# Kernel optimization log

Hardware: AMD Instinct MI355X
Metric: run time of the kernel (lower is better)

## Reference

```python
import jax, jax.numpy as jnp
import numpy as np
import math

HEADS = 4
LN_EPS = 1e-5


def _layer_norm(x, gamma, beta):
    # LayerNorm over last dim (N=4096), matching nn.LayerNorm(4096)
    mu = jnp.mean(x, axis=-1, keepdims=True)
    var = jnp.mean((x - mu) ** 2, axis=-1, keepdims=True)
    return (x - mu) * jax.lax.rsqrt(var + LN_EPS) * gamma + beta


def setup_inputs() -> dict:
    key = jax.random.key(0)
    ks = jax.random.split(key, 10)
    L, IMG, N = 1024, 1024, 4096
    s_img = 1.0 / math.sqrt(IMG)
    s_L = 1.0 / math.sqrt(L)
    return {
        "point_features": jax.random.normal(ks[0], (1, L, N), jnp.float32),
        "img_features": jax.random.normal(ks[1], (1, IMG, N), jnp.float32),
        # 4 per-head 1x1 convs IMG_chl -> L_chl
        "W_img": jax.random.normal(ks[2], (HEADS, L, IMG), jnp.float32) * s_img,
        "b_img": jax.random.normal(ks[3], (HEADS, L), jnp.float32) * s_img,
        # conv_L: L_chl -> L_chl
        "W_L": jax.random.normal(ks[4], (L, L), jnp.float32) * s_L,
        "b_L": jax.random.normal(ks[5], (L,), jnp.float32) * s_L,
        # LayerNorm(4096)
        "ln_g": jnp.ones((N,), jnp.float32),
        "ln_b": jnp.zeros((N,), jnp.float32),
        # conv_fusion: L_chl -> L_chl
        "W_f": jax.random.normal(ks[6], (L, L), jnp.float32) * s_L,
        "b_f": jax.random.normal(ks[7], (L,), jnp.float32) * s_L,
    }


def reference(point_features, img_features, W_img, b_img, W_L, b_L, ln_g, ln_b, W_f, b_f):
    # L_query = conv_L(point_features): [1, L, N]
    L_query = jnp.einsum('oi,bin->bon', W_L, point_features) + b_L[None, :, None]
    dk = L_query.shape[1]
    N = L_query.shape[2]

    # All 4 head keys at once: [H, 1, L, N]
    keys = jnp.einsum('hoi,bin->hbon', W_img, img_features) + b_img[:, None, :, None]

    # score_i = sum_c(key_i * query) / sqrt(dk)  -> cat over heads: [H, N] (B=1)
    score = jnp.sum(keys * L_query[None], axis=2).reshape(HEADS, N) / jnp.sqrt(jnp.float32(dk))

    # softmax across heads (dim=0), weightmap = [1, H, N]
    weight = jax.nn.softmax(score, axis=0)
    weightmap = weight[None]

    # z = sum_h weight[h] * key_h : [1, L, N]
    z = jnp.einsum('hn,hbcn->bcn', weight, keys)

    fused = _layer_norm(z + L_query, ln_g, ln_b)
    fusion_features = jnp.einsum('oi,bin->bon', W_f, fused) + b_f[None, :, None]
    return (fusion_features, weightmap)
```

## Files before the change

kernel.cpp:

```cpp
#include <hip/hip_runtime.h>
#include <hip/hip_bf16.h>
#include <stdint.h>

using u16 = unsigned short;

typedef __attribute__((ext_vector_type(8))) short bf16x8;
typedef __attribute__((ext_vector_type(4))) float f32x4;

typedef const __attribute__((address_space(1))) unsigned int* gas_t;
typedef __attribute__((address_space(3))) unsigned int* las_t;

__device__ inline void g2l16(const u16* g, u16* l) {
  __builtin_amdgcn_global_load_lds((gas_t)g, (las_t)l, 16, 0, 0);
}

__device__ inline u16 f2b(float x) {
  union { float f; uint32_t u; } v; v.f = x;
  uint32_t r = (v.u + 0x7FFFu + ((v.u >> 16) & 1u)) >> 16;
  return (u16)r;
}
__device__ inline float b2f(u16 b) {
  union { uint32_t u; float f; } v; v.u = ((uint32_t)b) << 16;
  return v.f;
}
__device__ inline float b2f_lo(uint32_t p) {
  union { uint32_t u; float f; } v; v.u = p << 16; return v.f;
}
__device__ inline float b2f_hi(uint32_t p) {
  union { uint32_t u; float f; } v; v.u = p & 0xFFFF0000u; return v.f;
}

__device__ inline void store_out(float* p, float v) { *p = v; }
__device__ inline void store_out(u16* p, float v) { *p = f2b(v); }

template<typename OutT>
__device__ inline void gemm_tile_128(const u16* __restrict__ A,
                                     const u16* __restrict__ Bt,
                                     const float* __restrict__ bias,
                                     OutT* __restrict__ C,
                                     int m0, int n0, int N, int K,
                                     u16* As, u16* Bs)
{
  const int tid  = threadIdx.x;
  const int wave = tid >> 6;
  const int lane = tid & 63;
  const int wm = wave >> 1, wn = wave & 1;
  const int lr = lane & 15;
  const int lq = lane >> 4;
  const int x7 = lr & 7;

  const int srow = tid >> 3;
  const int sgc  = (tid & 7) ^ (srow & 7);
  const u16* gA = A  + (size_t)(m0 + srow) * K + sgc * 8;
  const u16* gB = Bt + (size_t)(n0 + srow) * K + sgc * 8;
  u16* dstA = As + wave * 512;
  u16* dstB = Bs + wave * 512;

  f32x4 acc[4][4];
  #pragma unroll
  for (int i = 0; i < 4; ++i)
    #pragma unroll
    for (int j = 0; j < 4; ++j)
      acc[i][j] = (f32x4){0.f, 0.f, 0.f, 0.f};

  for (int k0 = 0; k0 < K; k0 += 64) {
    #pragma unroll
    for (int s = 0; s < 4; ++s) {
      g2l16(gA + (size_t)(s * 32) * K + k0, dstA + s * 2048);
      g2l16(gB + (size_t)(s * 32) * K + k0, dstB + s * 2048);
    }
    __syncthreads();

    #pragma unroll
    for (int ks = 0; ks < 2; ++ks) {
      const int pa = (ks * 4 + lq) ^ x7;
      bf16x8 af[4], bfr[4];
      #pragma unroll
      for (int im = 0; im < 4; ++im)
        af[im] = *(const bf16x8*)&As[(wm * 64 + im * 16 + lr) * 64 + pa * 8];
      #pragma unroll
      for (int in = 0; in < 4; ++in)
        bfr[in] = *(const bf16x8*)&Bs[(wn * 64 + in * 16 + lr) * 64 + pa * 8];

      #pragma unroll
      for (int im = 0; im < 4; ++im)
        #pragma unroll
        for (int in = 0; in < 4; ++in)
          acc[im][in] = __builtin_amdgcn_mfma_f32_16x16x32_bf16(
              af[im], bfr[in], acc[im][in], 0, 0, 0);
    }
    __syncthreads();
  }

  #pragma unroll
  for (int im = 0; im < 4; ++im) {
    const int mbase = m0 + wm * 64 + im * 16 + lq * 4;
    #pragma unroll
    for (int in = 0; in < 4; ++in) {
      const int ncol = n0 + wn * 64 + in * 16 + lr;
      #pragma unroll
      for (int r = 0; r < 4; ++r) {
        const int m = mbase + r;
        store_out(C + (size_t)m * N + ncol, acc[im][in][r] + bias[m]);
      }
    }
  }
}

__global__ __launch_bounds__(256)
void gemm_keys_q(const u16* __restrict__ WIb, const u16* __restrict__ IT,
                 const float* __restrict__ bim, u16* __restrict__ KEYS,
                 const u16* __restrict__ WLb, const u16* __restrict__ PT,
                 const float* __restrict__ bL, u16* __restrict__ Qb)
{
  __shared__ u16 As[128 * 64];
  __shared__ u16 Bs[128 * 64];
  const int by = blockIdx.y;
  const bool keys = (by < 32);
  const u16*   A    = keys ? WIb : WLb;
  const u16*   Bt   = keys ? IT  : PT;
  const float* bias = keys ? bim : bL;
  u16*         C    = keys ? KEYS : Qb;
  const int m0 = (by & 31) * 128;
  const int n0 = blockIdx.x * 128;
  gemm_tile_128<u16>(A, Bt, bias, C, m0, n0, 4096, 1024, As, Bs);
}

template<typename OutT>
__global__ __launch_bounds__(256)
void gemm_bt_64(const u16* __restrict__ A, const u16* __restrict__ Bt,
                const float* __restrict__ bias, OutT* __restrict__ C,
                int M, int N, int K)
{
  __shared__ u16 As[64 * 64];
  __shared__ u16 Bs[128 * 64];

  const int tid  = threadIdx.x;
  const int wave = tid >> 6;
  const int lane = tid & 63;
  const int lr = lane & 15;
  const int lq = lane >> 4;
  const int x7 = lr & 7;

  const int m0 = blockIdx.y * 64;
  const int n0 = blockIdx.x * 128;

  const int srow = tid >> 3;
  const int sgc  = (tid & 7) ^ (srow & 7);
  const u16* gA = A  + (size_t)(m0 + srow) * K + sgc * 8;
  const u16* gB = Bt + (size_t)(n0 + srow) * K + sgc * 8;
  u16* dstA = As + wave * 512;
  u16* dstB = Bs + wave * 512;

  f32x4 acc[4][2];
  #pragma unroll
  for (int i = 0; i < 4; ++i)
    #pragma unroll
    for (int j = 0; j < 2; ++j)
      acc[i][j] = (f32x4){0.f, 0.f, 0.f, 0.f};

  for (int k0 = 0; k0 < K; k0 += 64) {
    #pragma unroll
    for (int s = 0; s < 2; ++s)
      g2l16(gA + (size_t)(s * 32) * K + k0, dstA + s * 2048);
    #pragma unroll
    for (int s = 0; s < 4; ++s)
      g2l16(gB + (size_t)(s * 32) * K + k0, dstB + s * 2048);
    __syncthreads();

    #pragma unroll
    for (int ks = 0; ks < 2; ++ks) {
      const int pa = (ks * 4 + lq) ^ x7;
      bf16x8 af[4], bfr[2];
      #pragma unroll
      for (int im = 0; im < 4; ++im)
        af[im] = *(const bf16x8*)&As[(im * 16 + lr) * 64 + pa * 8];
      #pragma unroll
      for (int in = 0; in < 2; ++in)
        bfr[in] = *(const bf16x8*)&Bs[(wave * 32 + in * 16 + lr) * 64 + pa * 8];

      #pragma unroll
      for (int im = 0; im < 4; ++im)
        #pragma unroll
        for (int in = 0; in < 2; ++in)
          acc[im][in] = __builtin_amdgcn_mfma_f32_16x16x32_bf16(
              af[im], bfr[in], acc[im][in], 0, 0, 0);
    }
    __syncthreads();
  }

  #pragma unroll
  for (int im = 0; im < 4; ++im) {
    const int mbase = m0 + im * 16 + lq * 4;
    #pragma unroll
    for (int in = 0; in < 2; ++in) {
      const int ncol = n0 + wave * 32 + in * 16 + lr;
      #pragma unroll
      for (int r = 0; r < 4; ++r) {
        const int m = mbase + r;
        store_out(C + (size_t)m * N + ncol, acc[im][in][r] + bias[m]);
      }
    }
  }
}

__global__ __launch_bounds__(256)
void prep(const float* __restrict__ P, u16* __restrict__ PT,
          const float* __restrict__ I, u16* __restrict__ IT,
          const float4* __restrict__ wim, const float4* __restrict__ wl,
          const float4* __restrict__ wf, ushort4* __restrict__ wimb,
          ushort4* __restrict__ wlb, ushort4* __restrict__ wfb)
{
  const int bid = blockIdx.x;
  if (bid < 8192) {
    const int z   = bid >> 12;
    const int rem = bid & 4095;
    const int bx  = rem & 127;
    const int byy = rem >> 7;
    const float* in = z ? I : P;
    u16* out = z ? IT : PT;
    __shared__ u16 tile[32][33];
    const int c0 = bx * 32, r0 = byy * 32;
    const int tx = threadIdx.x & 31, ty = threadIdx.x >> 5;
    #pragma unroll
    for (int k = 0; k < 4; ++k)
      tile[ty + 8 * k][tx] = f2b(in[(size_t)(r0 + ty + 8 * k) * 4096 + c0 + tx]);
    __syncthreads();
    #pragma unroll
    for (int k = 0; k < 4; ++k)
      out[(size_t)(c0 + ty + 8 * k) * 1024 + r0 + tx] = tile[tx][ty + 8 * k];
  } else {
    int i = (bid - 8192) * 256 + threadIdx.x;
    const float4* src; ushort4* dst;
    if (i < 1048576)      { src = wim; dst = wimb; }
    else if (i < 1310720) { src = wl;  dst = wlb;  i -= 1048576; }
    else                  { src = wf;  dst = wfb;  i -= 1310720; }
    const float4 v = src[i];
    ushort4 o;
    o.x = f2b(v.x); o.y = f2b(v.y); o.z = f2b(v.z); o.w = f2b(v.w);
    dst[i] = o;
  }
}

__global__ __launch_bounds__(256)
void transpose_u16(const u16* __restrict__ in, u16* __restrict__ out,
                   int R, int C)
{
  __shared__ u16 tile[32][33];
  const int c0 = blockIdx.x * 32, r0 = blockIdx.y * 32;
  const int tx = threadIdx.x & 31, ty = threadIdx.x >> 5;
  #pragma unroll
  for (int k = 0; k < 4; ++k)
    tile[ty + 8 * k][tx] = in[(size_t)(r0 + ty + 8 * k) * C + c0 + tx];
  __syncthreads();
  #pragma unroll
  for (int k = 0; k < 4; ++k)
    out[(size_t)(c0 + ty + 8 * k) * R + r0 + tx] = tile[tx][ty + 8 * k];
}

__global__ __launch_bounds__(256)
void score_partial(const u16* __restrict__ keys, const u16* __restrict__ Qb,
                   float* __restrict__ score)
{
  const int n  = blockIdx.x * 256 + threadIdx.x;
  const int c0 = blockIdx.y * 32;
  float s[4] = {0.f, 0.f, 0.f, 0.f};
  for (int c = c0; c < c0 + 32; ++c) {
    const float q = b2f(Qb[(size_t)c * 4096 + n]);
    #pragma unroll
    for (int h = 0; h < 4; ++h)
      s[h] = fmaf(q, b2f(keys[((size_t)((h << 10) + c)) * 4096 + n]), s[h]);
  }
  #pragma unroll
  for (int h = 0; h < 4; ++h)
    atomicAdd(&score[h * 4096 + n], s[h] * 0.03125f);
}

__global__ __launch_bounds__(256)
void softmax_h(const float* __restrict__ score, float* __restrict__ wmap)
{
  const int n = blockIdx.x * 256 + threadIdx.x;
  const float s0 = score[n], s1 = score[4096 + n];
  const float s2 = score[8192 + n], s3 = score[12288 + n];
  const float m = fmaxf(fmaxf(s0, s1), fmaxf(s2, s3));
  const float e0 = expf(s0 - m), e1 = expf(s1 - m);
  const float e2 = expf(s2 - m), e3 = expf(s3 - m);
  const float inv = 1.f / (e0 + e1 + e2 + e3);
  wmap[n] = e0 * inv; wmap[4096 + n] = e1 * inv;
  wmap[8192 + n] = e2 * inv; wmap[12288 + n] = e3 * inv;
}

__global__ __launch_bounds__(256)
void z_ln(const u16* __restrict__ keys, const u16* __restrict__ Qb,
          const float* __restrict__ w, const float* __restrict__ g,
          const float* __restrict__ bb, u16* __restrict__ fused)
{
  const int c  = blockIdx.x;
  const int tx = threadIdx.x;
  float t[16];
  float s = 0.f, s2 = 0.f;
  #pragma unroll
  for (int j = 0; j < 2; ++j) {
    const int n = tx * 8 + j * 2048;
    const uint4 qv = *(const uint4*)&Qb[(size_t)c * 4096 + n];
    float z[8] = {0.f,0.f,0.f,0.f,0.f,0.f,0.f,0.f};
    #pragma unroll
    for (int h = 0; h < 4; ++h) {
      const uint4 kv = *(const uint4*)&keys[((size_t)((h << 10) + c)) * 4096 + n];
      const float4 w0 = *(const float4*)&w[h * 4096 + n];
      const float4 w1 = *(const float4*)&w[h * 4096 + n + 4];
      z[0] = fmaf(w0.x, b2f_lo(kv.x), z[0]);
      z[1] = fmaf(w0.y, b2f_hi(kv.x), z[1]);
      z[2] = fmaf(w0.z, b2f_lo(kv.y), z[2]);
      z[3] = fmaf(w0.w, b2f_hi(kv.y), z[3]);
      z[4] = fmaf(w1.x, b2f_lo(kv.z), z[4]);
      z[5] = fmaf(w1.y, b2f_hi(kv.z), z[5]);
      z[6] = fmaf(w1.z, b2f_lo(kv.w), z[6]);
      z[7] = fmaf(w1.w, b2f_hi(kv.w), z[7]);
    }
    const uint32_t qs[4] = {qv.x, qv.y, qv.z, qv.w};
    #pragma unroll
    for (int e = 0; e < 4; ++e) {
      const float v0 = z[2 * e]     + b2f_lo(qs[e]);
      const float v1 = z[2 * e + 1] + b2f_hi(qs[e]);
      t[8 * j + 2 * e]     = v0;
      t[8 * j + 2 * e + 1] = v1;
      s += v0 + v1;
      s2 = fmaf(v0, v0, fmaf(v1, v1, s2));
    }
  }
  #pragma unroll
  for (int o = 32; o > 0; o >>= 1) {
    s  += __shfl_down(s, o);
    s2 += __shfl_down(s2, o);
  }
  __shared__ float rbuf[8];
  const int wave = tx >> 6, lane = tx & 63;
  if (lane == 0) { rbuf[wave] = s; rbuf[4 + wave] = s2; }
  __syncthreads();
  s  = rbuf[0] + rbuf[1] + rbuf[2] + rbuf[3];
  s2 = rbuf[4] + rbuf[5] + rbuf[6] + rbuf[7];
  const float mu  = s * (1.f / 4096.f);
  const float var = s2 * (1.f / 4096.f) - mu * mu;
  const float rs  = rsqrtf(var + 1e-5f);
  #pragma unroll
  for (int j = 0; j < 2; ++j) {
    const int n = tx * 8 + j * 2048;
    #pragma unroll
    for (int q4 = 0; q4 < 2; ++q4) {
      const float4 gv = *(const float4*)&g[n + 4 * q4];
      const float4 bv = *(const float4*)&bb[n + 4 * q4];
      ushort4 o;
      o.x = f2b((t[8 * j + 4 * q4]     - mu) * rs * gv.x + bv.x);
      o.y = f2b((t[8 * j + 4 * q4 + 1] - mu) * rs * gv.y + bv.y);
      o.z = f2b((t[8 * j + 4 * q4 + 2] - mu) * rs * gv.z + bv.z);
      o.w = f2b((t[8 * j + 4 * q4 + 3] - mu) * rs * gv.w + bv.w);
      *(ushort4*)&fused[(size_t)c * 4096 + n + 4 * q4] = o;
    }
  }
}

extern "C" void kernel_launch(void* const* d_in, const int* in_sizes, int n_in,
                              void* d_out, int out_size, void* d_ws, size_t ws_size,
                              hipStream_t stream)
{
  const float* P   = (const float*)d_in[0];
  const float* I   = (const float*)d_in[1];
  const float* Wim = (const float*)d_in[2];
  const float* bim = (const float*)d_in[3];
  const float* WL  = (const float*)d_in[4];
  const float* bL  = (const float*)d_in[5];
  const float* lng = (const float*)d_in[6];
  const float* lnb = (const float*)d_in[7];
  const float* Wf  = (const float*)d_in[8];
  const float* bf_ = (const float*)d_in[9];
  float* out = (float*)d_out;

  char* ws = (char*)d_ws;
  u16*   PT     = (u16*)(ws + 0);
  u16*   IT     = (u16*)(ws + (size_t)8  * 1048576);
  u16*   WLb    = (u16*)(ws + (size_t)16 * 1048576);
  u16*   WIb    = (u16*)(ws + (size_t)18 * 1048576);
  u16*   WFb    = (u16*)(ws + (size_t)26 * 1048576);
  u16*   Qb     = (u16*)(ws + (size_t)28 * 1048576);
  u16*   KEYS   = (u16*)(ws + (size_t)36 * 1048576);
  float* SCORE  = (float*)(ws + (size_t)68 * 1048576);
  u16*   FUSED  = (u16*)(ws + (size_t)70 * 1048576);
  u16*   FUSEDT = (u16*)(ws + (size_t)78 * 1048576);

  const dim3 b256(256);

  prep<<<14336, b256, 0, stream>>>(P, PT, I, IT,
                                   (const float4*)Wim, (const float4*)WL,
                                   (const float4*)Wf, (ushort4*)WIb,
                                   (ushort4*)WLb, (ushort4*)WFb);

  gemm_keys_q<<<dim3(32, 40), b256, 0, stream>>>(WIb, IT, bim, KEYS,
                                                 WLb, PT, bL, Qb);

  hipMemsetAsync(SCORE, 0, 4 * 4096 * sizeof(float), stream);
  score_partial<<<dim3(16, 32), b256, 0, stream>>>(KEYS, Qb, SCORE);
  float* wmap = out + (size_t)1024 * 4096;
  softmax_h<<<16, b256, 0, stream>>>(SCORE, wmap);

  z_ln<<<1024, b256, 0, stream>>>(KEYS, Qb, wmap, lng, lnb, FUSED);
  transpose_u16<<<dim3(128, 32), b256, 0, stream>>>(FUSED, FUSEDT, 1024, 4096);

  gemm_bt_64<float><<<dim3(32, 16), b256, 0, stream>>>(WFb, FUSEDT, bf_, out, 1024, 4096, 1024);
}
```

Measured before the change: 210.4 us.

## Vectorize transposes with 64x64 tiles, fold score memset into prep, widen score loads

The fp32-to-bf16 input transposes and the FUSED transpose now use 64x64 tiles, with each thread moving 4x4 elements through float4/ushort4 loads and stores instead of scalar accesses. Zeroing the score buffer moves into extra blocks of the prep kernel, which removes the separate memset. score_partial now handles two columns per thread using 32-bit loads and splits channels into 16-wide chunks. This means twice as many atomic adds. It relies on helpers b2f_lo/b2f_hi that must exist in the hidden part of the file.

```diff
diff --git a/kernel.cpp b/kernel.cpp
--- a/kernel.cpp
+++ b/kernel.cpp
@@ -204,33 +204,79 @@
   }
 }
 
+__device__ inline void transpose_tile_f32(const float* __restrict__ in,
+                                          u16* __restrict__ out,
+                                          int R, int C, int r0, int c0)
+{
+  __shared__ u16 T[64 * 68];
+  const int tr = (threadIdx.x >> 4) * 4;
+  const int tc = (threadIdx.x & 15) * 4;
+  float4 v[4];
+  #pragma unroll
+  for (int i = 0; i < 4; ++i)
+    v[i] = *(const float4*)&in[(size_t)(r0 + tr + i) * C + c0 + tc];
+  #pragma unroll
+  for (int j = 0; j < 4; ++j) {
+    ushort4 o;
+    o.x = f2b(((const float*)&v[0])[j]);
+    o.y = f2b(((const float*)&v[1])[j]);
+    o.z = f2b(((const float*)&v[2])[j]);
+    o.w = f2b(((const float*)&v[3])[j]);
+    *(ushort4*)&T[(tc + j) * 68 + tr] = o;
+  }
+  __syncthreads();
+  #pragma unroll
+  for (int j = 0; j < 4; ++j) {
+    const ushort4 o = *(const ushort4*)&T[(tr + j) * 68 + tc];
+    *(ushort4*)&out[(size_t)(c0 + tr + j) * R + r0 + tc] = o;
+  }
+}
+
+__device__ inline void transpose_tile_u16(const u16* __restrict__ in,
+                                          u16* __restrict__ out,
+                                          int R, int C, int r0, int c0)
+{
+  __shared__ u16 T[64 * 68];
+  const int tr = (threadIdx.x >> 4) * 4;
+  const int tc = (threadIdx.x & 15) * 4;
+  ushort4 v[4];
+  #pragma unroll
+  for (int i = 0; i < 4; ++i)
+    v[i] = *(const ushort4*)&in[(size_t)(r0 + tr + i) * C + c0 + tc];
+  #pragma unroll
+  for (int j = 0; j < 4; ++j) {
+    ushort4 o;
+    o.x = ((const u16*)&v[0])[j];
+    o.y = ((const u16*)&v[1])[j];
+    o.z = ((const u16*)&v[2])[j];
+    o.w = ((const u16*)&v[3])[j];
+    *(ushort4*)&T[(tc + j) * 68 + tr] = o;
+  }
+  __syncthreads();
+  #pragma unroll
+  for (int j = 0; j < 4; ++j) {
+    const ushort4 o = *(const ushort4*)&T[(tr + j) * 68 + tc];
+    *(ushort4*)&out[(size_t)(c0 + tr + j) * R + r0 + tc] = o;
+  }
+}
+
 __global__ __launch_bounds__(256)
 void prep(const float* __restrict__ P, u16* __restrict__ PT,
           const float* __restrict__ I, u16* __restrict__ IT,
           const float4* __restrict__ wim, const float4* __restrict__ wl,
           const float4* __restrict__ wf, ushort4* __restrict__ wimb,
-          ushort4* __restrict__ wlb, ushort4* __restrict__ wfb)
+          ushort4* __restrict__ wlb, ushort4* __restrict__ wfb,
+          float4* __restrict__ score0)
 {
   const int bid = blockIdx.x;
-  if (bid < 8192) {
-    const int z   = bid >> 12;
-    const int rem = bid & 4095;
-    const int bx  = rem & 127;
-    const int byy = rem >> 7;
-    const float* in = z ? I : P;
-    u16* out = z ? IT : PT;
-    __shared__ u16 tile[32][33];
-    const int c0 = bx * 32, r0 = byy * 32;
-    const int tx = threadIdx.x & 31, ty = threadIdx.x >> 5;
-    #pragma unroll
-    for (int k = 0; k < 4; ++k)
-      tile[ty + 8 * k][tx] = f2b(in[(size_t)(r0 + ty + 8 * k) * 4096 + c0 + tx]);
-    __syncthreads();
-    #pragma unroll
-    for (int k = 0; k < 4; ++k)
-      out[(size_t)(c0 + ty + 8 * k) * 1024 + r0 + tx] = tile[tx][ty + 8 * k];
-  } else {
-    int i = (bid - 8192) * 256 + threadIdx.x;
+  if (bid < 2048) {
+    const int z   = bid >> 10;
+    const int rem = bid & 1023;
+    const int c0  = (rem & 63) * 64;
+    const int r0  = (rem >> 6) * 64;
+    transpose_tile_f32(z ? I : P, z ? IT : PT, 1024, 4096, r0, c0);
+  } else if (bid < 8192) {
+    int i = (bid - 2048) * 256 + threadIdx.x;
     const float4* src; ushort4* dst;
     if (i < 1048576)      { src = wim; dst = wimb; }
     else if (i < 1310720) { src = wl;  dst = wlb;  i -= 1048576; }
@@ -239,41 +285,43 @@
     ushort4 o;
     o.x = f2b(v.x); o.y = f2b(v.y); o.z = f2b(v.z); o.w = f2b(v.w);
     dst[i] = o;
-  }
-}
-
-__global__ __launch_bounds__(256)
-void transpose_u16(const u16* __restrict__ in, u16* __restrict__ out,
-                   int R, int C)
-{
-  __shared__ u16 tile[32][33];
-  const int c0 = blockIdx.x * 32, r0 = blockIdx.y * 32;
-  const int tx = threadIdx.x & 31, ty = threadIdx.x >> 5;
-  #pragma unroll
-  for (int k = 0; k < 4; ++k)
-    tile[ty + 8 * k][tx] = in[(size_t)(r0 + ty + 8 * k) * C + c0 + tx];
-  __syncthreads();
-  #pragma unroll
-  for (int k = 0; k < 4; ++k)
-    out[(size_t)(c0 + ty + 8 * k) * R + r0 + tx] = tile[tx][ty + 8 * k];
+  } else {
+    const int i = (bid - 8192) * 256 + threadIdx.x;
+    score0[i] = (float4){0.f, 0.f, 0.f, 0.f};
+  }
+}
+
+__global__ __launch_bounds__(256)
+void transpose_u16(const u16* __restrict__ in, u16* __restrict__ out)
+{
+  const int c0 = (blockIdx.x & 63) * 64;
+  const int r0 = (blockIdx.x >> 6) * 64;
+  transpose_tile_u16(in, out, 1024, 4096, r0, c0);
 }
 
 __global__ __launch_bounds__(256)
 void score_partial(const u16* __restrict__ keys, const u16* __restrict__ Qb,
                    float* __restrict__ score)
 {
-  const int n  = blockIdx.x * 256 + threadIdx.x;
-  const int c0 = blockIdx.y * 32;
-  float s[4] = {0.f, 0.f, 0.f, 0.f};
-  for (int c = c0; c < c0 + 32; ++c) {
-    const float q = b2f(Qb[(size_t)c * 4096 + n]);
-    #pragma unroll
-    for (int h = 0; h < 4; ++h)
-      s[h] = fmaf(q, b2f(keys[((size_t)((h << 10) + c)) * 4096 + n]), s[h]);
-  }
-  #pragma unroll
-  for (int h = 0; h < 4; ++h)
-    atomicAdd(&score[h * 4096 + n], s[h] * 0.03125f);
+  const int n  = (blockIdx.x * 256 + threadIdx.x) * 2;
+  const int c0 = blockIdx.y * 16;
+  float s0[4] = {0.f, 0.f, 0.f, 0.f};
+  float s1[4] = {0.f, 0.f, 0.f, 0.f};
+  for (int c = c0; c < c0 + 16; ++c) {
+    const uint32_t qv = *(const uint32_t*)&Qb[(size_t)c * 4096 + n];
+    const float q0 = b2f_lo(qv), q1 = b2f_hi(qv);
+    #pragma unroll
+    for (int h = 0; h < 4; ++h) {
+      const uint32_t kv = *(const uint32_t*)&keys[((size_t)((h << 10) + c)) * 4096 + n];
+      s0[h] = fmaf(q0, b2f_lo(kv), s0[h]);
+      s1[h] = fmaf(q1, b2f_hi(kv), s1[h]);
+    }
+  }
+  #pragma unroll
+  for (int h = 0; h < 4; ++h) {
+    atomicAdd(&score[h * 4096 + n],     s0[h] * 0.03125f);
+    atomicAdd(&score[h * 4096 + n + 1], s1[h] * 0.03125f);
+  }
 }
 
 __global__ __launch_bounds__(256)
@@ -390,21 +438,21 @@
 
   const dim3 b256(256);
 
-  prep<<<14336, b256, 0, stream>>>(P, PT, I, IT,
-                                   (const float4*)Wim, (const float4*)WL,
-                                   (const float4*)Wf, (ushort4*)WIb,
-                                   (ushort4*)WLb, (ushort4*)WFb);
+  prep<<<8208, b256, 0, stream>>>(P, PT, I, IT,
+                                  (const float4*)Wim, (const float4*)WL,
+                                  (const float4*)Wf, (ushort4*)WIb,
+                                  (ushort4*)WLb, (ushort4*)WFb,
+                                  (float4*)SCORE);
 
   gemm_keys_q<<<dim3(32, 40), b256, 0, stream>>>(WIb, IT, bim, KEYS,
                                                  WLb, PT, bL, Qb);
 
-  hipMemsetAsync(SCORE, 0, 4 * 4096 * sizeof(float), stream);
-  score_partial<<<dim3(16, 32), b256, 0, stream>>>(KEYS, Qb, SCORE);
+  score_partial<<<dim3(8, 64), b256, 0, stream>>>(KEYS, Qb, SCORE);
   float* wmap = out + (size_t)1024 * 4096;
   softmax_h<<<16, b256, 0, stream>>>(SCORE, wmap);
 
   z_ln<<<1024, b256, 0, stream>>>(KEYS, Qb, wmap, lng, lnb, FUSED);
-  transpose_u16<<<dim3(128, 32), b256, 0, stream>>>(FUSED, FUSEDT, 1024, 4096);
+  transpose_u16<<<1024, b256, 0, stream>>>(FUSED, FUSEDT);
 
   gemm_bt_64<float><<<dim3(32, 16), b256, 0, stream>>>(WFb, FUSEDT, bf_, out, 1024, 4096, 1024);
 }
```

New measurement: 212.0 us. No clear change (+0.8%).
